# Optimization experiments

Hardware: AMD Instinct MI355X
Metric: run time of the kernel (lower is better)

## Reference

```python
import jax, jax.numpy as jnp
import numpy as np
import math as m

Z_BOUNDS = (0.1, 1.0, 10.0)
STEPS = (128, 128)          # coarse samples per log-depth section
N_IMPORTANCE = 128          # fine samples (cfg.renderer.importance_steps)
ALPHA_RW = 1e-4             # cfg.renderer.alpha
INNER = 1.0                 # cfg.scene.inner_bound


def _uniform_z_log(n_rays):
    segs = []
    for i in range(len(STEPS)):
        lo, hi = m.log10(Z_BOUNDS[i]), m.log10(Z_BOUNDS[i + 1])
        segs.append(jnp.linspace(lo, hi - (hi - lo) / STEPS[i], STEPS[i], dtype=jnp.float32))
    zl = jnp.concatenate(segs)
    return jnp.broadcast_to(zl, (n_rays, zl.shape[0]))


def _contract(x):
    # mipnerf360-style contraction (helpers.mipnerf360_scale)
    x = x / INNER
    n = jnp.maximum(jnp.linalg.norm(x, axis=-1, keepdims=True), 1e-8)
    return jnp.where(n <= 1.0, x, (2.0 - 1.0 / n) * x / n)


def _density(s):
    # analytic stand-in for the abstract density() network
    return 25.0 * jnp.exp(-4.0 * jnp.sum(s * s, axis=-1))


def _radiance(s, d):
    # analytic stand-in for the abstract forward(x, d)
    return _density(s), jax.nn.sigmoid(s + 0.1 * d)


def _weights_from_sigma(sig, zl):
    # delta in log-depth space; last delta = 0 (so last alpha = 0), as in source
    delta = jnp.concatenate([zl[:, 1:] - zl[:, :-1], jnp.zeros_like(zl[:, :1])], axis=-1)
    alpha = 1.0 - jnp.exp(-sig * delta)
    alpha_shift = jnp.concatenate([jnp.zeros_like(alpha[:, :1]), alpha[:, :-1]], axis=-1)
    trans = jnp.cumprod(1.0 - alpha_shift, axis=-1)
    return alpha * trans


def _reweight(w):
    S = w.shape[-1]
    wp = jnp.pad(w, ((0, 0), (1, 1)))
    w = 0.5 * (jnp.maximum(wp[:, :-2], wp[:, 1:-1]) + jnp.maximum(wp[:, 1:-1], wp[:, 2:]))
    w = w + ALPHA_RW / S
    scale = jnp.concatenate([jnp.full((s_,), s_ / sum(STEPS), dtype=jnp.float32) for s_ in STEPS])
    w = w * scale
    return w / jnp.sum(w, axis=-1, keepdims=True)


def _sample_pdf(bins, weights, n):
    # inverse-CDF importance sampling (helpers.sample_pdf), deterministic stratified u
    pdf = weights / jnp.sum(weights, axis=-1, keepdims=True)
    cdf = jnp.cumsum(pdf, axis=-1)                     # [N, S]
    u = (jnp.arange(n, dtype=jnp.float32) + 0.5) / n
    u = jnp.broadcast_to(u, (bins.shape[0], n))
    inds = jax.vmap(lambda c, uu: jnp.searchsorted(c, uu, side='right'))(cdf, u)
    S = bins.shape[-1]
    below = jnp.clip(inds - 1, 0, S - 1)
    above = jnp.clip(inds, 0, S - 1)
    tg = lambda a, i: jnp.take_along_axis(a, i, axis=-1)
    c0, c1 = tg(cdf, below), tg(cdf, above)
    b0, b1 = tg(bins, below), tg(bins, above)
    denom = jnp.where(c1 - c0 < 1e-8, 1.0, c1 - c0)
    t = jnp.clip((u - c0) / denom, 0.0, 1.0)
    return b0 + t * (b1 - b0)


def setup_inputs():
    key = jax.random.key(0)
    k1, k2, k3 = jax.random.split(key, 3)
    N = 65536
    rays_o = 0.1 * jax.random.normal(k1, (N, 3), jnp.float32)
    rays_d = jax.random.normal(k2, (N, 3), jnp.float32)
    bg_color = jax.random.uniform(k3, (3,), jnp.float32)
    return {"rays_o": rays_o, "rays_d": rays_d, "bg_color": bg_color}


def reference(rays_o, rays_d, bg_color):
    rays_d = rays_d / jnp.linalg.norm(rays_d, axis=-1, keepdims=True)
    N = rays_o.shape[0]
    # --- efficient_sampling (torch.no_grad in source) ---
    zl = _uniform_z_log(N)                             # [N, 256]
    z = 10.0 ** zl
    xyz = rays_o[:, None, :] + rays_d[:, None, :] * z[..., None]   # [N, 256, 3]
    sig = _density(_contract(xyz))
    w = _weights_from_sigma(sig, zl)
    w_re = _reweight(w)
    zlf = jax.lax.stop_gradient(_sample_pdf(zl, w_re, N_IMPORTANCE))  # [N, 128]
    zf = 10.0 ** zlf
    # --- render ---
    xyzf = rays_o[:, None, :] + rays_d[:, None, :] * zf[..., None]    # [N, 128, 3]
    dirs = jnp.broadcast_to(rays_d[:, None, :], xyzf.shape)
    sigf, rgbf = _radiance(_contract(xyzf), dirs)
    wf = _weights_from_sigma(sigf, zlf)
    image = jnp.einsum('ns,nsc->nc', wf, rgbf)
    invdepth = jnp.sum(wf / zf, axis=-1)
    image = image + (1.0 - jnp.sum(wf, axis=-1))[:, None] * bg_color
    lo, hi = m.log10(Z_BOUNDS[0]), m.log10(Z_BOUNDS[-1])
    z_vals_log_s = (zlf - lo) / (hi - lo)
    return image, wf, z_vals_log_s, invdepth
```

## Files before the change

### kernel.cpp

```cpp
#include <hip/hip_runtime.h>

#define WPB 4
#define BLOCK (64 * WPB)
#define SC 256
#define SF 128

typedef float v2f __attribute__((ext_vector_type(2)));
typedef float v4f __attribute__((ext_vector_type(4)));

__device__ __forceinline__ float fexp2(float x) {
#if __has_builtin(__builtin_amdgcn_exp2f)
    return __builtin_amdgcn_exp2f(x);
#else
    return exp2f(x);
#endif
}
__device__ __forceinline__ float frcp(float x) {
#if __has_builtin(__builtin_amdgcn_rcpf)
    return __builtin_amdgcn_rcpf(x);
#else
    return 1.0f / x;
#endif
}
__device__ __forceinline__ float frsq(float x) {
#if __has_builtin(__builtin_amdgcn_rsqf)
    return __builtin_amdgcn_rsqf(x);
#else
    return rsqrtf(x);
#endif
}

#define DPPF(oldv, x, ctrl, rmask, bc)                                          \
    __int_as_float(__builtin_amdgcn_update_dpp(                                 \
        __float_as_int(oldv), __float_as_int(x), (ctrl), (rmask), 0xf, (bc)))

#define ROW_SHR1   0x111
#define ROW_SHR2   0x112
#define ROW_SHR4   0x114
#define ROW_SHR8   0x118
#define WAVE_SHL1  0x130
#define WAVE_SHR1  0x138
#define ROW_BC15   0x142
#define ROW_BC31   0x143

__device__ __forceinline__ float scan_mul_incl(float x) {
    x *= DPPF(1.0f, x, ROW_SHR1, 0xf, false);
    x *= DPPF(1.0f, x, ROW_SHR2, 0xf, false);
    x *= DPPF(1.0f, x, ROW_SHR4, 0xf, false);
    x *= DPPF(1.0f, x, ROW_SHR8, 0xf, false);
    x *= DPPF(1.0f, x, ROW_BC15, 0xa, false);
    x *= DPPF(1.0f, x, ROW_BC31, 0xc, false);
    return x;
}
__device__ __forceinline__ float scan_add_incl(float x) {
    x += DPPF(0.0f, x, ROW_SHR1, 0xf, true);
    x += DPPF(0.0f, x, ROW_SHR2, 0xf, true);
    x += DPPF(0.0f, x, ROW_SHR4, 0xf, true);
    x += DPPF(0.0f, x, ROW_SHR8, 0xf, true);
    x += DPPF(0.0f, x, ROW_BC15, 0xa, true);
    x += DPPF(0.0f, x, ROW_BC31, 0xc, true);
    return x;
}
__device__ __forceinline__ float readlanef(float x, int l) {
    return __int_as_float(__builtin_amdgcn_readlane(__float_as_int(x), l));
}

__global__ __launch_bounds__(BLOCK, 8) void nerf_render(
    const float* __restrict__ rays_o, const float* __restrict__ rays_d,
    const float* __restrict__ bgp, float* __restrict__ out, int N) {
    const int wid  = __builtin_amdgcn_readfirstlane(threadIdx.x >> 6);
    const int lane = threadIdx.x & 63;
    const int ray  = __builtin_amdgcn_readfirstlane(blockIdx.x * WPB + wid);
    __shared__ float cdf_s[WPB][SC];

    const float L2_10 = 3.3219280948873623f;
    const float L2_E  = 1.4426950408889634f;
    const float DLT   = 0.0078125f;
    const float C2  = -4.0f * L2_E;
    const float C1  = -L2_E * 25.0f * DLT;
    const float C25 = -L2_E * 25.0f;
    const float CADD = 1e-4f / 256.0f;

    float ox = rays_o[ray * 3 + 0], oy = rays_o[ray * 3 + 1], oz = rays_o[ray * 3 + 2];
    float dx = rays_d[ray * 3 + 0], dy = rays_d[ray * 3 + 1], dz = rays_d[ray * 3 + 2];
    {
        float rn = frsq(dx * dx + dy * dy + dz * dz);
        dx *= rn; dy *= rn; dz *= rn;
    }
    float dxn = dx * (-0.1f * L2_E), dyn = dy * (-0.1f * L2_E), dzn = dz * (-0.1f * L2_E);

    float zl0 = -1.0f + (float)(lane << 2) * DLT;
    float z0  = fexp2(zl0 * L2_10);
    v2f zz[2];
    zz[0].x = z0;                          zz[0].y = z0 * 1.0181517217011025f;
    zz[1].x = z0 * 1.0366329284377645f;    zz[1].y = z0 * 1.0554494416179205f;

    v2f ee[2];
#pragma unroll
    for (int p = 0; p < 2; p++) {
        v2f z  = zz[p];
        v2f px = dx * z + ox, py = dy * z + oy, pz = dz * z + oz;
        v2f nsq = px * px + py * py + pz * pz;
        v2f rn; rn.x = frsq(nsq.x); rn.y = frsq(nsq.y);
        v2f t2 = 2.0f - rn;
        v2f fs = t2 * t2;
        v2f ssq;
        ssq.x = nsq.x > 1.0f ? fs.x : nsq.x;
        ssq.y = nsq.y > 1.0f ? fs.y : nsq.y;
        v2f sr = C2 * ssq;
        v2f sg; sg.x = fexp2(sr.x); sg.y = fexp2(sr.y);
        v2f ea = C1 * sg;
        ee[p].x = fexp2(ea.x); ee[p].y = fexp2(ea.y);
    }
    if (lane == 63) ee[1].y = 1.0f;

    float lp  = (ee[0].x * ee[0].y) * (ee[1].x * ee[1].y);
    float tp  = scan_mul_incl(lp);
    float tin = DPPF(1.0f, tp, WAVE_SHR1, 0xf, false);

    v2f om0 = 1.0f - ee[0], om1 = 1.0f - ee[1];
    float c1 = ee[0].x, c2 = c1 * ee[0].y, c3 = c2 * ee[1].x;
    v2f t01; t01.x = tin;      t01.y = tin * c1;
    v2f t23; t23.x = tin * c2; t23.y = tin * c3;
    v2f w01 = om0 * t01, w23 = om1 * t23;

    float wprev = DPPF(0.0f, w23.y, WAVE_SHR1, 0xf, false);
    float wnext = DPPF(0.0f, w01.x, WAVE_SHL1, 0xf, false);
    float m0 = fmaxf(wprev, w01.x), m1 = fmaxf(w01.x, w01.y),
          m2 = fmaxf(w01.y, w23.x), m3 = fmaxf(w23.x, w23.y),
          m4 = fmaxf(w23.y, wnext);
    float wr0 = 0.5f * (m0 + m1) + CADD, wr1 = 0.5f * (m1 + m2) + CADD,
          wr2 = 0.5f * (m2 + m3) + CADD, wr3 = 0.5f * (m3 + m4) + CADD;

    float s0 = wr0, s1 = s0 + wr1, s2 = s1 + wr2, s3 = s2 + wr3;
    float incl = scan_add_incl(s3);
    float exb  = DPPF(0.0f, incl, WAVE_SHR1, 0xf, true);
    float invT = frcp(readlanef(incl, 63));
    v2f cdfa; cdfa.x = (exb + s0) * invT; cdfa.y = (exb + s1) * invT;
    v2f cdfb; cdfb.x = (exb + s2) * invT; cdfb.y = (exb + s3) * invT;
    *(v2f*)&cdf_s[wid][(lane << 2) + 0] = cdfa;
    *(v2f*)&cdf_s[wid][(lane << 2) + 2] = cdfb;
    const float* cdf = cdf_s[wid];

    const float p63  = readlanef(cdfb.y, 15);
    const float p127 = readlanef(cdfb.y, 31);
    const float p191 = readlanef(cdfb.y, 47);

    float zlf[2], zvs[2];
    float ubase = (float)lane * 0.015625f;
#pragma unroll
    for (int jj = 0; jj < 2; jj++) {
        float u = ubase + (jj ? 0.01171875f : 0.00390625f);
        int base = (((int)(p63 <= u) + (int)(p127 <= u) + (int)(p191 <= u)) << 6);
        {
            float qa = cdf[base + 15], qb = cdf[base + 31], qc = cdf[base + 47];
            base += (((int)(qa <= u) + (int)(qb <= u) + (int)(qc <= u)) << 4);
        }
        {
            float ra_ = cdf[base + 3], rb_ = cdf[base + 7], rc_ = cdf[base + 11];
            base += (((int)(ra_ <= u) + (int)(rb_ <= u) + (int)(rc_ <= u)) << 2);
        }
        v4f r = *(const v4f*)(cdf + base);
        int bm1 = base - 1;
        float cm1 = cdf[bm1 < 0 ? 0 : bm1];
        bool le0 = (r.x <= u), le1 = (r.y <= u), le2 = (r.z <= u);
        int cnt  = (int)le0 + (int)le1 + (int)le2;
        float c1v = le2 ? r.w : (le1 ? r.z : (le0 ? r.y : r.x));
        float c0  = le2 ? r.z : (le1 ? r.y : (le0 ? r.x : cm1));
        float t = (u - c0) * frcp(c1v - c0);
        float f = fmaxf((float)(bm1 + cnt) + t, 0.0f);
        zlf[jj] = fmaf(DLT, f, -1.0f);
        zvs[jj] = f * 0.00390625f;
    }

    float zlf2 = DPPF(zlf[1], zlf[0], WAVE_SHL1, 0xf, false);
    v2f del; del.x = zlf[1] - zlf[0]; del.y = zlf2 - zlf[1];
    v2f zf;  zf.x = fexp2(zlf[0] * L2_10); zf.y = fexp2(zlf[1] * L2_10);
    float zq  = zf.x * zf.y;
    float rzq = frcp(zq);
    v2f invz; invz.x = rzq * zf.y; invz.y = rzq * zf.x;
    v2f px = dx * zf + ox, py = dy * zf + oy, pz = dz * zf + oz;
    v2f nsq = px * px + py * py + pz * pz;
    v2f rn; rn.x = frsq(nsq.x); rn.y = frsq(nsq.y);
    v2f t2 = 2.0f - rn;
    v2f fs = t2 * t2;
    v2f fcl = (rn * t2) * (-L2_E);
    v2f ssq, facL;
    ssq.x = nsq.x > 1.0f ? fs.x : nsq.x;  facL.x = nsq.x > 1.0f ? fcl.x : -L2_E;
    ssq.y = nsq.y > 1.0f ? fs.y : nsq.y;  facL.y = nsq.y > 1.0f ? fcl.y : -L2_E;
    v2f sr = C2 * ssq;
    v2f sg; sg.x = fexp2(sr.x); sg.y = fexp2(sr.y);
    v2f ea = (C25 * sg) * del;
    v2f ef; ef.x = fexp2(ea.x); ef.y = fexp2(ea.y);

    v2f axr = px * facL + dxn;
    v2f axg = py * facL + dyn;
    v2f axb = pz * facL + dzn;
    v2f er; er.x = fexp2(axr.x); er.y = fexp2(axr.y);
    v2f eg; eg.x = fexp2(axg.x); eg.y = fexp2(axg.y);
    v2f eb; eb.x = fexp2(axb.x); eb.y = fexp2(axb.y);
    v2f dr = 1.0f + er, dg = 1.0f + eg, db = 1.0f + eb;
    v2f m_rg = dr * dg;
    v2f m_gb = dg * db;
    v2f m_rb = dr * db;
    v2f P    = m_rg * db;
    v2f rp; rp.x = frcp(P.x); rp.y = frcp(P.y);
    v2f rv = rp * m_gb;
    v2f gv = rp * m_rb;
    v2f bv = rp * m_rg;

    float tpf  = scan_mul_incl(ef.x * ef.y);
    float tinf = DPPF(1.0f, tpf, WAVE_SHR1, 0xf, false);
    float Ttot = readlanef(tpf, 63);
    float wf0 = (1.0f - ef.x) * tinf;
    float wf1 = (1.0f - ef.y) * (tinf * ef.x);
    v2f wfv; wfv.x = wf0; wfv.y = wf1;

    v2f pr = wfv * rv, pg = wfv * gv, pb = wfv * bv, pi = wfv * invz;
    float ar = scan_add_incl(pr.x + pr.y);
    float ag = scan_add_incl(pg.x + pg.y);
    float ab = scan_add_incl(pb.x + pb.y);
    float ai = scan_add_incl(pi.x + pi.y);

    const unsigned NN = (unsigned)N;
    float* wf_base  = out + 3u * NN;
    float* zvs_base = wf_base + NN * (unsigned)SF;
    float* inv_base = zvs_base + NN * (unsigned)SF;
    unsigned col = (unsigned)ray * (unsigned)SF + (unsigned)(lane << 1);
    *(float2*)(wf_base + col) = make_float2(wf0, wf1);
    *(float2*)(zvs_base + col) = make_float2(zvs[0], zvs[1]);
    if (lane == 63) {
        out[(unsigned)ray * 3u + 0u] = fmaf(Ttot, bgp[0], ar);
        out[(unsigned)ray * 3u + 1u] = fmaf(Ttot, bgp[1], ag);
        out[(unsigned)ray * 3u + 2u] = fmaf(Ttot, bgp[2], ab);
        inv_base[(unsigned)ray] = ai;
    }
}

extern "C" void kernel_launch(void* const* d_in, const int* in_sizes, int n_in,
                              void* d_out, int out_size, void* d_ws, size_t ws_size,
                              hipStream_t stream) {
    const float* rays_o = (const float*)d_in[0];
    const float* rays_d = (const float*)d_in[1];
    const float* bg     = (const float*)d_in[2];
    float* out = (float*)d_out;
    int N = in_sizes[0] / 3;
    int blocks = (N + WPB - 1) / WPB;
    nerf_render<<<blocks, BLOCK, 0, stream>>>(rays_o, rays_d, bg, out, N);
}
```

Measured before the change: 115.1 us.

## Replace per-sample CDF tree search with LDS histogram and prefix-sum scan

Each fine sample used to run a multi-level 4-ary search over the shared CDF. Now each CDF entry is binned by which stratified u-slot it falls into, using LDS atomics into a per-wave histogram. A wave-level integer prefix scan of the histogram then gives each sample's searchsorted index directly. This drops the dependent chain of LDS reads and comparisons, at the cost of LDS atomics, an extra shared array, and the ceil-based binning having to match searchsorted exactly at boundaries.

```diff
diff --git a/kernel.cpp b/kernel.cpp
--- a/kernel.cpp
+++ b/kernel.cpp
@@ -4,6 +4,7 @@
 #define BLOCK (64 * WPB)
 #define SC 256
 #define SF 128
+#define NB 132
 
 typedef float v2f __attribute__((ext_vector_type(2)));
 typedef float v4f __attribute__((ext_vector_type(4)));
@@ -61,6 +62,15 @@
     x += DPPF(0.0f, x, ROW_BC31, 0xc, true);
     return x;
 }
+__device__ __forceinline__ int scan_add_incl_i(int x) {
+    x += __builtin_amdgcn_update_dpp(0, x, ROW_SHR1, 0xf, 0xf, true);
+    x += __builtin_amdgcn_update_dpp(0, x, ROW_SHR2, 0xf, 0xf, true);
+    x += __builtin_amdgcn_update_dpp(0, x, ROW_SHR4, 0xf, 0xf, true);
+    x += __builtin_amdgcn_update_dpp(0, x, ROW_SHR8, 0xf, 0xf, true);
+    x += __builtin_amdgcn_update_dpp(0, x, ROW_BC15, 0xa, 0xf, true);
+    x += __builtin_amdgcn_update_dpp(0, x, ROW_BC31, 0xc, 0xf, true);
+    return x;
+}
 __device__ __forceinline__ float readlanef(float x, int l) {
     return __int_as_float(__builtin_amdgcn_readlane(__float_as_int(x), l));
 }
@@ -72,6 +82,7 @@
     const int lane = threadIdx.x & 63;
     const int ray  = __builtin_amdgcn_readfirstlane(blockIdx.x * WPB + wid);
     __shared__ float cdf_s[WPB][SC];
+    __shared__ int   hist_s[WPB][NB];
 
     const float L2_10 = 3.3219280948873623f;
     const float L2_E  = 1.4426950408889634f;
@@ -142,33 +153,35 @@
     *(v2f*)&cdf_s[wid][(lane << 2) + 2] = cdfb;
     const float* cdf = cdf_s[wid];
 
-    const float p63  = readlanef(cdfb.y, 15);
-    const float p127 = readlanef(cdfb.y, 31);
-    const float p191 = readlanef(cdfb.y, 47);
+    {
+        int2 z2; z2.x = 0; z2.y = 0;
+        *(int2*)&hist_s[wid][lane << 1] = z2;
+    }
+    {
+        int jm;
+        jm = (int)ceilf(fmaf(cdfa.x, 128.0f, -0.5f)); atomicAdd(&hist_s[wid][jm], 1);
+        jm = (int)ceilf(fmaf(cdfa.y, 128.0f, -0.5f)); atomicAdd(&hist_s[wid][jm], 1);
+        jm = (int)ceilf(fmaf(cdfb.x, 128.0f, -0.5f)); atomicAdd(&hist_s[wid][jm], 1);
+        jm = (int)ceilf(fmaf(cdfb.y, 128.0f, -0.5f)); atomicAdd(&hist_s[wid][jm], 1);
+    }
+    int2 hp = *(int2*)&hist_s[wid][lane << 1];
+    int inclh = scan_add_incl_i(hp.x + hp.y);
+    int indsA[2];
+    indsA[0] = inclh - hp.y;
+    indsA[1] = inclh;
 
     float zlf[2], zvs[2];
     float ubase = (float)lane * 0.015625f;
 #pragma unroll
     for (int jj = 0; jj < 2; jj++) {
         float u = ubase + (jj ? 0.01171875f : 0.00390625f);
-        int base = (((int)(p63 <= u) + (int)(p127 <= u) + (int)(p191 <= u)) << 6);
-        {
-            float qa = cdf[base + 15], qb = cdf[base + 31], qc = cdf[base + 47];
-            base += (((int)(qa <= u) + (int)(qb <= u) + (int)(qc <= u)) << 4);
-        }
-        {
-            float ra_ = cdf[base + 3], rb_ = cdf[base + 7], rc_ = cdf[base + 11];
-            base += (((int)(ra_ <= u) + (int)(rb_ <= u) + (int)(rc_ <= u)) << 2);
-        }
-        v4f r = *(const v4f*)(cdf + base);
-        int bm1 = base - 1;
-        float cm1 = cdf[bm1 < 0 ? 0 : bm1];
-        bool le0 = (r.x <= u), le1 = (r.y <= u), le2 = (r.z <= u);
-        int cnt  = (int)le0 + (int)le1 + (int)le2;
-        float c1v = le2 ? r.w : (le1 ? r.z : (le0 ? r.y : r.x));
-        float c0  = le2 ? r.z : (le1 ? r.y : (le0 ? r.x : cm1));
+        int inds = indsA[jj];
+        int im1  = inds - 1;
+        int ia   = im1 < 0 ? 0 : im1;
+        float c0  = cdf[ia];
+        float c1v = cdf[ia + 1];
         float t = (u - c0) * frcp(c1v - c0);
-        float f = fmaxf((float)(bm1 + cnt) + t, 0.0f);
+        float f = fmaxf((float)im1 + t, 0.0f);
         zlf[jj] = fmaf(DLT, f, -1.0f);
         zvs[jj] = f * 0.00390625f;
     }
```

Result: slower. 126.1 us (+9.6%).
